# Kernel tuning notes

Measured on AMD Instinct MI355X. Metric: run time of the kernel, lower is better.

The kernel has to match this reference:

```python
import jax, jax.numpy as jnp
import numpy as np
from jax import lax

# Fixed Sobel kernels, OIHW layout: [2 out, 1 in, 3, 3]
_GX = np.array([[1, 0, -1], [2, 0, -2], [1, 0, -1]], dtype=np.float32)
_GY = np.array([[1, 2, 1], [0, 0, 0], [-1, -2, -1]], dtype=np.float32)
SOBEL_K = jnp.asarray(np.stack([_GX, _GY], 0)[:, None])  # [2,1,3,3]


def setup_inputs() -> dict:
    key = jax.random.key(0)
    x = jax.random.normal(key, (16, 1, 1024, 1024), dtype=jnp.float32)
    return {"x": x}


def reference(x):
    # Sobel conv, padding=1 (SAME): y [B,2,H,W]
    y = lax.conv_general_dilated(
        x, SOBEL_K, window_strides=(1, 1), padding=((1, 1), (1, 1)),
        dimension_numbers=("NCHW", "OIHW", "NCHW"))
    # sb_x: cross-correlation with [1,-1] along W -> s[:, :-1] - s[:, 1:], then drop last row
    s0 = jnp.sign(y[:, 0:1])                       # [B,1,H,W]
    y0 = (s0[..., :-1] - s0[..., 1:])[..., :-1, :]  # [B,1,H-1,W-1]
    # sb_y: cross-correlation with [1,-1]^T along H -> s[:-1] - s[1:], then drop last col
    s1 = jnp.sign(y[:, 1:2])                       # [B,1,H,W]
    y1 = (s1[..., :-1, :] - s1[..., 1:, :])[..., :-1]  # [B,1,H-1,W-1]
    return (y, y0, y1)
```

## Files before the change

kernel.cpp:

```cpp
#include <hip/hip_runtime.h>


struct Row7 { double v[7]; };

__device__ __forceinline__ Row7 load_row(const float* __restrict__ xb, int r, int t) {
    Row7 o;
    int rc = min(max(r, 0), 1023);
    float m = ((unsigned)r < 1024u) ? 1.0f : 0.0f;
    const float4* __restrict__ rp = (const float4*)(xb + (rc << 10));
    float4 L = rp[(t > 0) ? (t - 1) : 0];
    float4 C = rp[t];
    float4 R = rp[(t < 255) ? (t + 1) : 255];
    float lw = (t > 0)   ? L.w : 0.0f;
    float r0 = (t < 255) ? R.x : 0.0f;
    float r1 = (t < 255) ? R.y : 0.0f;
    o.v[0] = (double)(lw  * m);
    o.v[1] = (double)(C.x * m);
    o.v[2] = (double)(C.y * m);
    o.v[3] = (double)(C.z * m);
    o.v[4] = (double)(C.w * m);
    o.v[5] = (double)(r0  * m);
    o.v[6] = (double)(r1  * m);
    return o;
}

__device__ __forceinline__ float fsign(double v) {
    return (v > 0.0) ? 1.0f : ((v < 0.0) ? -1.0f : 0.0f);
}

__global__ __launch_bounds__(256) void sobel_sign_kernel(const float* __restrict__ x,
                                                         float* __restrict__ out) {
    const int t  = threadIdx.x;
    const int bh = blockIdx.x;
    const int b  = bh >> 10;
    const int h  = bh & 1023;
    const int w0 = t << 2;
    const float* __restrict__ xb = x + ((size_t)b << 20);

    Row7 A0 = load_row(xb, h - 1, t);
    Row7 A1 = load_row(xb, h,     t);
    Row7 A2 = load_row(xb, h + 1, t);

    double tc[7], d[6];
    #pragma unroll
    for (int c = 0; c < 7; ++c) tc[c] = A0.v[c] + 2.0 * A1.v[c] + A2.v[c];
    #pragma unroll
    for (int c = 0; c < 6; ++c) d[c] = A0.v[c] - A2.v[c];

    Row7 A3 = load_row(xb, h + 2, t);
    double e[6];
    #pragma unroll
    for (int c = 0; c < 6; ++c) e[c] = A1.v[c] - A3.v[c];

    double gx0[4], gx1[4], gy0[4], gy1[4];
    #pragma unroll
    for (int j = 0; j < 4; ++j) {
        gx0[j] = tc[j]     - tc[j + 2];
        gx1[j] = tc[j + 1] - tc[j + 3];
        gy0[j] = d[j] + 2.0 * d[j + 1] + d[j + 2];
        gy1[j] = e[j] + 2.0 * e[j + 1] + e[j + 2];
    }

    float4 vgx = make_float4((float)gx0[0], (float)gx0[1], (float)gx0[2], (float)gx0[3]);
    float4 vgy = make_float4((float)gy0[0], (float)gy0[1], (float)gy0[2], (float)gy0[3]);
    size_t ybase = ((size_t)b << 21) + ((size_t)h << 10) + (size_t)w0;
    *(float4*)(out + ybase)               = vgx;
    *(float4*)(out + ybase + (1u << 20))  = vgy;

    if (h < 1023) {
        const size_t NP = (size_t)1023 * 1023;
        size_t p = (size_t)33554432u + (size_t)b * NP + (size_t)h * 1023u + (size_t)w0;
        #pragma unroll
        for (int j = 0; j < 4; ++j) {
            if (w0 + j < 1023) {
                out[p + j]             = fsign(gx0[j]) - fsign(gx1[j]);
                out[p + j + 16744464u] = fsign(gy0[j]) - fsign(gy1[j]);
            }
        }
    }
}

extern "C" void kernel_launch(void* const* d_in, const int* in_sizes, int n_in,
                              void* d_out, int out_size, void* d_ws, size_t ws_size,
                              hipStream_t stream) {
    const float* x = (const float*)d_in[0];
    float* out = (float*)d_out;
    dim3 grid(16 * 1024), block(256);
    sobel_sign_kernel<<<grid, block, 0, stream>>>(x, out);
}
```

Baseline: 364.3 us.

## Process eight rows per block with rolling row registers and reuse computed signs

Each block now handles eight consecutive rows instead of one, keeping a rotating three-row register window so every input row is loaded about once per block rather than four times. The gx sign difference comes from five gx values in the same row, and the gy sign difference reuses the previous row's signs, which removes the redundant second Sobel evaluation. The grid shrinks eightfold, which lowers parallelism to 2048 blocks and raises register use for the unrolled loop.

```diff
diff --git a/kernel.cpp b/kernel.cpp
--- a/kernel.cpp
+++ b/kernel.cpp
@@ -1,10 +1,8 @@
 #include <hip/hip_runtime.h>
 
 
-struct Row7 { double v[7]; };
-
-__device__ __forceinline__ Row7 load_row(const float* __restrict__ xb, int r, int t) {
-    Row7 o;
+__device__ __forceinline__ void load_row(const float* __restrict__ xb, int r, int t,
+                                         double* __restrict__ o ) {
     int rc = min(max(r, 0), 1023);
     float m = ((unsigned)r < 1024u) ? 1.0f : 0.0f;
     const float4* __restrict__ rp = (const float4*)(xb + (rc << 10));
@@ -14,14 +12,13 @@
     float lw = (t > 0)   ? L.w : 0.0f;
     float r0 = (t < 255) ? R.x : 0.0f;
     float r1 = (t < 255) ? R.y : 0.0f;
-    o.v[0] = (double)(lw  * m);
-    o.v[1] = (double)(C.x * m);
-    o.v[2] = (double)(C.y * m);
-    o.v[3] = (double)(C.z * m);
-    o.v[4] = (double)(C.w * m);
-    o.v[5] = (double)(r0  * m);
-    o.v[6] = (double)(r1  * m);
-    return o;
+    o[0] = (double)(lw  * m);
+    o[1] = (double)(C.x * m);
+    o[2] = (double)(C.y * m);
+    o[3] = (double)(C.z * m);
+    o[4] = (double)(C.w * m);
+    o[5] = (double)(r0  * m);
+    o[6] = (double)(r1  * m);
 }
 
 __device__ __forceinline__ float fsign(double v) {
@@ -31,51 +28,85 @@
 __global__ __launch_bounds__(256) void sobel_sign_kernel(const float* __restrict__ x,
                                                          float* __restrict__ out) {
     const int t  = threadIdx.x;
-    const int bh = blockIdx.x;
-    const int b  = bh >> 10;
-    const int h  = bh & 1023;
+    const int b  = blockIdx.x >> 7;
+    const int hg = blockIdx.x & 127;
+    const int h0 = hg << 3;
     const int w0 = t << 2;
+
     const float* __restrict__ xb = x + ((size_t)b << 20);
+    float* __restrict__ yb = out + ((size_t)b << 21);
+    const size_t NP    = (size_t)1023 * 1023;
+    const size_t Y0    = 33554432u + (size_t)b * NP;
+    const size_t Y1    = 50298896u + (size_t)b * NP;
 
-    Row7 A0 = load_row(xb, h - 1, t);
-    Row7 A1 = load_row(xb, h,     t);
-    Row7 A2 = load_row(xb, h + 1, t);
+    double r[3][7];
+    load_row(xb, h0 - 1, t, r[0]);
+    load_row(xb, h0,     t, r[1]);
 
-    double tc[7], d[6];
+    float psgy[4];
+
     #pragma unroll
-    for (int c = 0; c < 7; ++c) tc[c] = A0.v[c] + 2.0 * A1.v[c] + A2.v[c];
-    #pragma unroll
-    for (int c = 0; c < 6; ++c) d[c] = A0.v[c] - A2.v[c];
+    for (int it = 0; it < 8; ++it) {
+        const int h = h0 + it;
+        double* A0 = r[it % 3];
+        double* A1 = r[(it + 1) % 3];
+        double* A2 = r[(it + 2) % 3];
+        load_row(xb, h + 1, t, A2);
 
-    Row7 A3 = load_row(xb, h + 2, t);
-    double e[6];
-    #pragma unroll
-    for (int c = 0; c < 6; ++c) e[c] = A1.v[c] - A3.v[c];
+        double tc[7], d[6];
+        #pragma unroll
+        for (int c = 0; c < 7; ++c) tc[c] = A0[c] + 2.0 * A1[c] + A2[c];
+        #pragma unroll
+        for (int c = 0; c < 6; ++c) d[c] = A0[c] - A2[c];
 
-    double gx0[4], gx1[4], gy0[4], gy1[4];
-    #pragma unroll
-    for (int j = 0; j < 4; ++j) {
-        gx0[j] = tc[j]     - tc[j + 2];
-        gx1[j] = tc[j + 1] - tc[j + 3];
-        gy0[j] = d[j] + 2.0 * d[j + 1] + d[j + 2];
-        gy1[j] = e[j] + 2.0 * e[j + 1] + e[j + 2];
+        double gx[5];
+        #pragma unroll
+        for (int j = 0; j < 5; ++j) gx[j] = tc[j] - tc[j + 2];
+        double gy[4];
+        #pragma unroll
+        for (int j = 0; j < 4; ++j) gy[j] = d[j] + 2.0 * d[j + 1] + d[j + 2];
+
+        size_t yo = ((size_t)h << 10) + (size_t)w0;
+        *(float4*)(yb + yo) =
+            make_float4((float)gx[0], (float)gx[1], (float)gx[2], (float)gx[3]);
+        *(float4*)(yb + yo + (1u << 20)) =
+            make_float4((float)gy[0], (float)gy[1], (float)gy[2], (float)gy[3]);
+
+        float sgx[5], sgy[4];
+        #pragma unroll
+        for (int j = 0; j < 5; ++j) sgx[j] = fsign(gx[j]);
+        #pragma unroll
+        for (int j = 0; j < 4; ++j) sgy[j] = fsign(gy[j]);
+
+        if (h < 1023) {
+            size_t p = Y0 + (size_t)h * 1023u + (size_t)w0;
+            #pragma unroll
+            for (int j = 0; j < 4; ++j)
+                if (w0 + j < 1023) out[p + j] = sgx[j] - sgx[j + 1];
+        }
+        if (it > 0) {
+            size_t p = Y1 + (size_t)(h - 1) * 1023u + (size_t)w0;
+            #pragma unroll
+            for (int j = 0; j < 4; ++j)
+                if (w0 + j < 1023) out[p + j] = psgy[j] - sgy[j];
+        }
+        #pragma unroll
+        for (int j = 0; j < 4; ++j) psgy[j] = sgy[j];
     }
 
-    float4 vgx = make_float4((float)gx0[0], (float)gx0[1], (float)gx0[2], (float)gx0[3]);
-    float4 vgy = make_float4((float)gy0[0], (float)gy0[1], (float)gy0[2], (float)gy0[3]);
-    size_t ybase = ((size_t)b << 21) + ((size_t)h << 10) + (size_t)w0;
-    *(float4*)(out + ybase)               = vgx;
-    *(float4*)(out + ybase + (1u << 20))  = vgy;
-
-    if (h < 1023) {
-        const size_t NP = (size_t)1023 * 1023;
-        size_t p = (size_t)33554432u + (size_t)b * NP + (size_t)h * 1023u + (size_t)w0;
+    const int hl = h0 + 7;
+    if (hl < 1023) {
+        double* B0 = r[8 % 3];
+        double bn[7];
+        load_row(xb, hl + 2, t, bn);
+        double d2[6];
+        #pragma unroll
+        for (int c = 0; c < 6; ++c) d2[c] = B0[c] - bn[c];
+        size_t p = Y1 + (size_t)hl * 1023u + (size_t)w0;
         #pragma unroll
         for (int j = 0; j < 4; ++j) {
-            if (w0 + j < 1023) {
-                out[p + j]             = fsign(gx0[j]) - fsign(gx1[j]);
-                out[p + j + 16744464u] = fsign(gy0[j]) - fsign(gy1[j]);
-            }
+            double gyn = d2[j] + 2.0 * d2[j + 1] + d2[j + 2];
+            if (w0 + j < 1023) out[p + j] = psgy[j] - fsign(gyn);
         }
     }
 }
@@ -85,6 +116,6 @@
                               hipStream_t stream) {
     const float* x = (const float*)d_in[0];
     float* out = (float*)d_out;
-    dim3 grid(16 * 1024), block(256);
+    dim3 grid(16 * 128), block(256);
     sobel_sign_kernel<<<grid, block, 0, stream>>>(x, out);
 }
```

Result: faster. 354.7 us (-2.6%).
